# Kernel tuning notes

Measured on AMD Instinct MI355X. Metric: run time of the kernel, lower is better.

## Reference

```python
import jax, jax.numpy as jnp
import numpy as np

NUM_HEADS = 16
D_MODEL = 1024
NUM_LAYERS = 4
VOCAB = 32000
SEQ_LEN = 1024
BATCH = 4
EPS = 1e-6


def position_embedding(seq_len, d_model):
    pos = jnp.arange(seq_len, dtype=jnp.float32)[:, None]
    i = jnp.arange(d_model, dtype=jnp.float32)[None, :]
    # faithful to source: angle_rates = 1 / (1/10000)^(2*(i//2)/d) = 10000^(2*(i//2)/d)
    angle_rates = jnp.power(10000.0, 2.0 * jnp.floor(i / 2.0) / float(d_model))
    ang = pos * angle_rates  # [S, D]
    return jnp.concatenate([jnp.sin(ang[:, 0::2]), jnp.cos(ang[:, 1::2])], axis=-1)[None]  # [1,S,D]


def layer_norm(x, g, b):
    m = jnp.mean(x, axis=-1, keepdims=True)
    v = jnp.mean(jnp.square(x - m), axis=-1, keepdims=True)
    return (x - m) * jax.lax.rsqrt(v + EPS) * g + b


def setup_inputs() -> dict:
    key = jax.random.key(0)
    ks = jax.random.split(key, 20)
    L, D = NUM_LAYERS, D_MODEL
    s = 0.02
    inp = {
        "x": jax.random.randint(ks[0], (BATCH, SEQ_LEN), 0, VOCAB, dtype=jnp.int32),
        "mask": jnp.zeros((BATCH, 1, 1, SEQ_LEN), dtype=jnp.float32),
        "emb": jax.random.normal(ks[1], (VOCAB, D), dtype=jnp.float32) * s,
        "wq": jax.random.normal(ks[2], (L, D, D), dtype=jnp.float32) * s,
        "bq": jnp.zeros((L, D), dtype=jnp.float32),
        "wk": jax.random.normal(ks[3], (L, D, D), dtype=jnp.float32) * s,
        "bk": jnp.zeros((L, D), dtype=jnp.float32),
        "wv": jax.random.normal(ks[4], (L, D, D), dtype=jnp.float32) * s,
        "bv": jnp.zeros((L, D), dtype=jnp.float32),
        "wo": jax.random.normal(ks[5], (L, D, D), dtype=jnp.float32) * s,
        "bo": jnp.zeros((L, D), dtype=jnp.float32),
        "wf": jax.random.normal(ks[6], (L, D, D), dtype=jnp.float32) * s,
        "bf": jnp.zeros((L, D), dtype=jnp.float32),
        "g1": jnp.ones((L, D), dtype=jnp.float32),
        "b1": jnp.zeros((L, D), dtype=jnp.float32),
        "g2": jnp.ones((L, D), dtype=jnp.float32),
        "b2": jnp.zeros((L, D), dtype=jnp.float32),
    }
    return inp


def encoder_forward(x, mask, emb, wq, bq, wk, bk, wv, bv, wo, bo, wf, bf, g1, b1, g2, b2):
    B, S = x.shape
    D = emb.shape[1]
    H = NUM_HEADS
    dh = D // H
    h = emb[x] * jnp.sqrt(jnp.float32(D))  # [B,S,D]
    h = h + position_embedding(S, D)[:, :S, :]

    def split_heads(t):  # [B,S,D] -> [B,H,S,dh]
        return t.reshape(B, S, H, dh).transpose(0, 2, 1, 3)

    for l in range(wq.shape[0]):
        q = split_heads(h @ wq[l] + bq[l])
        k = split_heads(h @ wk[l] + bk[l])
        v = split_heads(h @ wv[l] + bv[l])
        scores = jnp.einsum("bhqd,bhkd->bhqk", q, k) / jnp.sqrt(jnp.float32(dh))
        scores = scores + mask * -1e9
        w = jax.nn.softmax(scores, axis=-1)
        ctx = jnp.einsum("bhqk,bhkd->bhqd", w, v)  # [B,H,S,dh]
        ctx = ctx.transpose(0, 2, 1, 3).reshape(B, S, D)
        attn_out = ctx @ wo[l] + bo[l]
        h = layer_norm(h + attn_out, g1[l], b1[l])
        ff = h @ wf[l] + bf[l]
        h = layer_norm(h + ff, g2[l], b2[l])
    return h


def reference(x, mask, emb, wq, bq, wk, bk, wv, bv, wo, bo, wf, bf, g1, b1, g2, b2):
    return encoder_forward(x, mask, emb, wq, bq, wk, bk, wv, bv, wo, bo, wf, bf, g1, b1, g2, b2)
```

## Files before the change

kernel.cpp:

```cpp
#include <hip/hip_runtime.h>
#include <hip/hip_bf16.h>
#include <math.h>

typedef __hip_bfloat16 bf16;
typedef unsigned int u32;
typedef __attribute__((ext_vector_type(8))) short short8;
typedef __attribute__((ext_vector_type(4))) float f32x4;


#define ATT_LDK 72
#define PS_LD  72

typedef __attribute__((address_space(3))) u32 lds_u32;
typedef const __attribute__((address_space(1))) u32 glb_u32;
static __device__ __forceinline__ void g2l16(const void* g, void* l) {
    __builtin_amdgcn_global_load_lds((glb_u32*)g, (lds_u32*)l, 16, 0, 0);
}

static __device__ __forceinline__ unsigned short bf16bits(float f) {
    bf16 h = __float2bfloat16(f);
    return *(unsigned short*)&h;
}

__global__ __launch_bounds__(256) void wprep_kernel(
    const float* __restrict__ wq, const float* __restrict__ wk,
    const float* __restrict__ wv, const float* __restrict__ wo,
    const float* __restrict__ wf, bf16* __restrict__ wt_all)
{
    __shared__ bf16 tile[64][ATT_LDK];
    const int z = blockIdx.z;
    const int l = z / 5, f = z % 5;
    const float* src = (f == 0) ? wq : (f == 1) ? wk : (f == 2) ? wv : (f == 3) ? wo : wf;
    src += (size_t)l * 1024 * 1024;
    bf16* dst = wt_all + ((size_t)l * 5 + f) * 1024 * 1024;

    const int k0 = blockIdx.x * 64, n0 = blockIdx.y * 64;
    const int t = threadIdx.x;
#pragma unroll
    for (int rr = 0; rr < 4; ++rr) {
        int slot = t + rr * 256;
        int r = slot >> 4, c = slot & 15;
        float4 v = *(const float4*)(src + (size_t)(k0 + r) * 1024 + n0 + c * 4);
        tile[c * 4 + 0][r] = __float2bfloat16(v.x);
        tile[c * 4 + 1][r] = __float2bfloat16(v.y);
        tile[c * 4 + 2][r] = __float2bfloat16(v.z);
        tile[c * 4 + 3][r] = __float2bfloat16(v.w);
    }
    __syncthreads();
#pragma unroll
    for (int rr = 0; rr < 2; ++rr) {
        int slot = t + rr * 256;
        int n = slot >> 3, c = slot & 7;
        *(uint4*)(dst + (size_t)(n0 + n) * 1024 + k0 + c * 8) = *(const uint4*)&tile[n][c * 8];
    }
}

__global__ void bias_stack_kernel(const float* __restrict__ bq, const float* __restrict__ bk,
                                  const float* __restrict__ bv, float* __restrict__ bqkv)
{
    int i = blockIdx.x * 256 + threadIdx.x;
    if (i < 4 * 3072) {
        int l = i / 3072, c = i % 3072;
        int fam = c >> 10, cc = c & 1023;
        const float* s = (fam == 0) ? bq : (fam == 1) ? bk : bv;
        bqkv[i] = s[l * 1024 + cc];
    }
}

__global__ __launch_bounds__(256) void embed_kernel(
    const int* __restrict__ x, const float* __restrict__ emb,
    float* __restrict__ hf, bf16* __restrict__ hb)
{
    int idx = blockIdx.x * 256 + threadIdx.x;
    int d0 = (idx & 255) * 4;
    int row = idx >> 8;
    int s = row & 1023;
    int tok = x[row];
    float4 e = *(const float4*)(emb + (size_t)tok * 1024 + d0);
    float vv[4] = {e.x, e.y, e.z, e.w};
    float out[4];
#pragma unroll
    for (int j = 0; j < 4; ++j) {
        int d = d0 + j;
        int m = (d < 512) ? d : (d - 512);
        float ex = (float)(2 * m) * (1.0f / 1024.0f);
        float rate = (float)pow(10000.0, (double)ex);
        float ang = (float)s * rate;
        double a = (double)ang;
        float pe = (d < 512) ? (float)sin(a) : (float)cos(a);
        out[j] = vv[j] * 32.0f + pe;
    }
    *(float4*)(hf + (size_t)row * 1024 + d0) = *(float4*)out;
    unsigned short pk[4];
#pragma unroll
    for (int j = 0; j < 4; ++j) pk[j] = bf16bits(out[j]);
    *(uint2*)(hb + (size_t)row * 1024 + d0) = *(uint2*)pk;
}

__global__ __launch_bounds__(256, 2) void gemm_bt_kernel(
    const bf16* __restrict__ A, const bf16* __restrict__ Bt,
    const float* __restrict__ bias,
    float* __restrict__ Cf, bf16* __restrict__ Cb,
    int M, int N, int K)
{
    __shared__ bf16 As[128 * 32];
    __shared__ bf16 Bs[128 * 32];
    __shared__ bf16 Cst[4][16 * PS_LD];
    const int t = threadIdx.x;
    const int lane = t & 63, wave = t >> 6;
    const int wr = wave >> 1, wc = wave & 1;
    const int lidx = lane & 15, quad = lane >> 4;
    const int m0 = blockIdx.x * 128, n0 = blockIdx.y * 128;

    f32x4 acc[4][4];
#pragma unroll
    for (int i = 0; i < 4; ++i)
#pragma unroll
        for (int j = 0; j < 4; ++j) acc[i][j] = (f32x4){0.f, 0.f, 0.f, 0.f};

    const int r0 = wave * 32;
    const int rloc = lane >> 2;
    const int csw = ((lane & 3) ^ ((lane >> 3) & 3)) * 8;
    const bf16* Abase = A  + (size_t)(m0 + r0 + rloc) * K + csw;
    const bf16* Bbase = Bt + (size_t)(n0 + r0 + rloc) * K + csw;
    bf16* AsW = As + r0 * 32;
    bf16* BsW = Bs + r0 * 32;
    const int aslot = (quad ^ ((lidx >> 1) & 3)) * 8;

    for (int k0 = 0; k0 < K; k0 += 32) {
        __syncthreads();
        g2l16(Abase + k0,                  AsW);
        g2l16(Abase + k0 + 16 * (size_t)K, AsW + 16 * 32);
        g2l16(Bbase + k0,                  BsW);
        g2l16(Bbase + k0 + 16 * (size_t)K, BsW + 16 * 32);
        __syncthreads();

        short8 af[4], bfr[4];
#pragma unroll
        for (int i = 0; i < 4; ++i)
            af[i] = *(const short8*)(As + (wr * 64 + i * 16 + lidx) * 32 + aslot);
#pragma unroll
        for (int j = 0; j < 4; ++j)
            bfr[j] = *(const short8*)(Bs + (wc * 64 + j * 16 + lidx) * 32 + aslot);
#pragma unroll
        for (int i = 0; i < 4; ++i)
#pragma unroll
            for (int j = 0; j < 4; ++j)
                acc[i][j] = __builtin_amdgcn_mfma_f32_16x16x32_bf16(af[i], bfr[j], acc[i][j], 0, 0, 0);
    }

    float bvj[4];
#pragma unroll
    for (int j = 0; j < 4; ++j)
        bvj[j] = bias ? bias[n0 + wc * 64 + j * 16 + lidx] : 0.0f;

    if (Cb) {
        const int row16 = lane >> 2, c4 = lane & 3;
#pragma unroll
        for (int i = 0; i < 4; ++i) {
#pragma unroll
            for (int j = 0; j < 4; ++j)
#pragma unroll
                for (int r = 0; r < 4; ++r)
                    Cst[wave][(quad * 4 + r) * PS_LD + j * 16 + lidx] =
                        __float2bfloat16(acc[i][j][r] + bvj[j]);
            bf16* dst = Cb + (size_t)(m0 + wr * 64 + i * 16 + row16) * N + n0 + wc * 64;
            const bf16* srcr = &Cst[wave][row16 * PS_LD];
#pragma unroll
            for (int h = 0; h < 2; ++h)
                *(uint4*)(dst + (c4 + 4 * h) * 8) = *(const uint4*)(srcr + (c4 + 4 * h) * 8);
        }
    } else {
#pragma unroll
        for (int i = 0; i < 4; ++i)
#pragma unroll
            for (int j = 0; j < 4; ++j) {
                int col = n0 + wc * 64 + j * 16 + lidx;
#pragma unroll
                for (int r = 0; r < 4; ++r) {
                    int rowg = m0 + wr * 64 + i * 16 + quad * 4 + r;
                    Cf[(size_t)rowg * N + col] = acc[i][j][r] + bvj[j];
                }
            }
    }
}

__global__ __launch_bounds__(256) void transpose_v_kernel(
    const bf16* __restrict__ QKV, bf16* __restrict__ Vt)
{
    __shared__ bf16 tile[64][ATT_LDK];
    const int t = threadIdx.x;
    const int s0 = blockIdx.x * 64, d0 = blockIdx.y * 64, b = blockIdx.z;
#pragma unroll
    for (int rr = 0; rr < 2; ++rr) {
        int slot = t + rr * 256;
        int sl = slot >> 3, c = slot & 7;
        bf16 tmp[8];
        *(uint4*)tmp = *(const uint4*)(QKV + (size_t)(b * 1024 + s0 + sl) * 3072 + 2048 + d0 + c * 8);
#pragma unroll
        for (int j = 0; j < 8; ++j) tile[c * 8 + j][sl] = tmp[j];
    }
    __syncthreads();
#pragma unroll
    for (int rr = 0; rr < 2; ++rr) {
        int slot = t + rr * 256;
        int dl = slot >> 3, c = slot & 7;
        *(uint4*)(Vt + (size_t)(b * 1024 + d0 + dl) * 1024 + s0 + c * 8) = *(const uint4*)&tile[dl][c * 8];
    }
}

__global__ __launch_bounds__(512, 4) void attention_kernel(
    const bf16* __restrict__ QKV,
    const bf16* __restrict__ Vt,
    const float* __restrict__ mask,
    bf16* __restrict__ ctx)
{
    __shared__ bf16 Ks[64 * 64];
    __shared__ bf16 Vs[64 * 64];
    __shared__ bf16 Ps[8][16 * PS_LD];

    const int t = threadIdx.x, lane = t & 63, wave = t >> 6;
    const int quad = lane >> 4, lidx = lane & 15;
    const int b = blockIdx.x >> 4, hh = blockIdx.x & 15;
    const int q0 = blockIdx.y * 128 + wave * 16;

    const int r8 = lane >> 3;
    const int gc = ((lane & 7) ^ r8) * 8;
    const bf16* kg0 = QKV + (size_t)(b * 1024 + wave * 8 + r8) * 3072 + 1024 + hh * 64 + gc;
    const bf16* vg0 = Vt  + (size_t)(b * 1024 + hh * 64 + wave * 8 + r8) * 1024 + gc;
    bf16* KsW = Ks + wave * 8 * 64;
    bf16* VsW = Vs + wave * 8 * 64;

    short8 qf[2];
    {
        const bf16* qp = QKV + (size_t)(b * 1024 + q0 + lidx) * 3072 + hh * 64;
        qf[0] = *(const short8*)(qp + quad * 8);
        qf[1] = *(const short8*)(qp + 32 + quad * 8);
    }

    f32x4 Oacc[4];
#pragma unroll
    for (int nt = 0; nt < 4; ++nt) Oacc[nt] = (f32x4){0.f, 0.f, 0.f, 0.f};
    float psum[4] = {0.f, 0.f, 0.f, 0.f};

    const int fslot = lidx & 7;

    for (int kt = 0; kt < 16; ++kt) {
        __syncthreads();
        g2l16(kg0 + (size_t)kt * 64 * 3072, KsW);
        g2l16(vg0 + kt * 64, VsW);
        __syncthreads();

        f32x4 sacc[4];
#pragma unroll
        for (int nt = 0; nt < 4; ++nt) sacc[nt] = (f32x4){0.f, 0.f, 0.f, 0.f};
#pragma unroll
        for (int kk = 0; kk < 2; ++kk)
#pragma unroll
            for (int nt = 0; nt < 4; ++nt) {
                short8 kf = *(const short8*)(Ks + (nt * 16 + lidx) * 64 + (((kk * 4 + quad) ^ fslot) * 8));
                sacc[nt] = __builtin_amdgcn_mfma_f32_16x16x32_bf16(qf[kk], kf, sacc[nt], 0, 0, 0);
            }

#pragma unroll
        for (int nt = 0; nt < 4; ++nt) {
            float mv = mask[b * 1024 + kt * 64 + nt * 16 + lidx] * -1e9f;
#pragma unroll
            for (int r = 0; r < 4; ++r) {
                float p = __expf(sacc[nt][r] * 0.125f + mv);
                sacc[nt][r] = p;
                psum[r] += p;
            }
        }

#pragma unroll
        for (int nt = 0; nt < 4; ++nt)
#pragma unroll
            for (int r = 0; r < 4; ++r)
                Ps[wave][(quad * 4 + r) * PS_LD + nt * 16 + lidx] = __float2bfloat16(sacc[nt][r]);

#pragma unroll
        for (int kk = 0; kk < 2; ++kk) {
            short8 pf = *(const short8*)(&Ps[wave][lidx * PS_LD + kk * 32 + quad * 8]);
#pragma unroll
            for (int nt = 0; nt < 4; ++nt) {
                short8 vf = *(const short8*)(Vs + (nt * 16 + lidx) * 64 + (((kk * 4 + quad) ^ fslot) * 8));
                Oacc[nt] = __builtin_amdgcn_mfma_f32_16x16x32_bf16(pf, vf, Oacc[nt], 0, 0, 0);
            }
        }
    }

#pragma unroll
    for (int off = 1; off < 16; off <<= 1)
#pragma unroll
        for (int r = 0; r < 4; ++r)
            psum[r] += __shfl_xor(psum[r], off, 64);
    float linv[4];
#pragma unroll
    for (int r = 0; r < 4; ++r) linv[r] = 1.0f / psum[r];

#pragma unroll
    for (int nt = 0; nt < 4; ++nt)
#pragma unroll
        for (int r = 0; r < 4; ++r)
            Ps[wave][(quad * 4 + r) * PS_LD + nt * 16 + lidx] = __float2bfloat16(Oacc[nt][r] * linv[r]);

    const int row16 = lane >> 2, c4 = lane & 3;
    bf16* dst = ctx + (size_t)(b * 1024 + q0 + row16) * 1024 + hh * 64;
    const bf16* srcr = &Ps[wave][row16 * PS_LD];
#pragma unroll
    for (int h = 0; h < 2; ++h)
        *(uint4*)(dst + (c4 + 4 * h) * 8) = *(const uint4*)(srcr + (c4 + 4 * h) * 8);
}

__global__ __launch_bounds__(256) void add_ln_kernel(
    const float* __restrict__ x, const float* __restrict__ dx,
    const float* __restrict__ g, const float* __restrict__ b,
    float* __restrict__ outf, bf16* __restrict__ outb)
{
    __shared__ float red[4];
    const int row = blockIdx.x;
    const int t = threadIdx.x;
    const int c0 = t * 4;
    float4 xv = *(const float4*)(x + (size_t)row * 1024 + c0);
    float4 dv = *(const float4*)(dx + (size_t)row * 1024 + c0);
    float v[4] = {xv.x + dv.x, xv.y + dv.y, xv.z + dv.z, xv.w + dv.w};
    float s = v[0] + v[1] + v[2] + v[3];
#pragma unroll
    for (int off = 1; off < 64; off <<= 1) s += __shfl_xor(s, off, 64);
    if ((t & 63) == 0) red[t >> 6] = s;
    __syncthreads();
    float mean = (red[0] + red[1] + red[2] + red[3]) * (1.0f / 1024.0f);
    float sq = 0.f;
#pragma unroll
    for (int i = 0; i < 4; ++i) { float d = v[i] - mean; sq += d * d; }
#pragma unroll
    for (int off = 1; off < 64; off <<= 1) sq += __shfl_xor(sq, off, 64);
    __syncthreads();
    if ((t & 63) == 0) red[t >> 6] = sq;
    __syncthreads();
    float var = (red[0] + red[1] + red[2] + red[3]) * (1.0f / 1024.0f);
    float rs = rsqrtf(var + 1e-6f);
    float4 gv = *(const float4*)(g + c0);
    float4 bv = *(const float4*)(b + c0);
    float gg[4] = {gv.x, gv.y, gv.z, gv.w}, bb[4] = {bv.x, bv.y, bv.z, bv.w};
    float o[4];
    unsigned short pk[4];
#pragma unroll
    for (int i = 0; i < 4; ++i) {
        o[i] = (v[i] - mean) * rs * gg[i] + bb[i];
        pk[i] = bf16bits(o[i]);
    }
    *(float4*)(outf + (size_t)row * 1024 + c0) = *(float4*)o;
    *(uint2*)(outb + (size_t)row * 1024 + c0) = *(uint2*)pk;
}

extern "C" void kernel_launch(void* const* d_in, const int* in_sizes, int n_in,
                              void* d_out, int out_size, void* d_ws, size_t ws_size,
                              hipStream_t stream)
{
    const int*   x    = (const int*)d_in[0];
    const float* mask = (const float*)d_in[1];
    const float* emb  = (const float*)d_in[2];
    const float* wq   = (const float*)d_in[3];
    const float* bq   = (const float*)d_in[4];
    const float* wk   = (const float*)d_in[5];
    const float* bk   = (const float*)d_in[6];
    const float* wv   = (const float*)d_in[7];
    const float* bv   = (const float*)d_in[8];
    const float* wo   = (const float*)d_in[9];
    const float* bo   = (const float*)d_in[10];
    const float* wf   = (const float*)d_in[11];
    const float* bfp  = (const float*)d_in[12];
    const float* g1   = (const float*)d_in[13];
    const float* b1   = (const float*)d_in[14];
    const float* g2   = (const float*)d_in[15];
    const float* b2   = (const float*)d_in[16];

    char* ws = (char*)d_ws;
    float* h_f  = (float*)ws;                 ws += 4096ull * 1024 * 4;
    bf16*  h_b  = (bf16*)ws;                  ws += 4096ull * 1024 * 2;
    bf16*  qkv  = (bf16*)ws;                  ws += 4096ull * 3072 * 2;
    bf16*  vt   = (bf16*)ws;                  ws += 4096ull * 1024 * 2;
    bf16*  ctx  = (bf16*)ws;                  ws += 4096ull * 1024 * 2;
    bf16*  wt   = (bf16*)ws;                  ws += 20ull * 1024 * 1024 * 2;
    float* bqkv = (float*)ws;                 ws += 4ull * 3072 * 4;
    float* delta = (float*)qkv;

    wprep_kernel<<<dim3(16, 16, 20), 256, 0, stream>>>(wq, wk, wv, wo, wf, wt);
    bias_stack_kernel<<<dim3(48), 256, 0, stream>>>(bq, bk, bv, bqkv);
    embed_kernel<<<dim3(4096), 256, 0, stream>>>(x, emb, h_f, h_b);

    for (int l = 0; l < 4; ++l) {
        bf16* wt_l = wt + (size_t)l * 5 * 1024 * 1024;
        gemm_bt_kernel<<<dim3(32, 24), 256, 0, stream>>>(
            h_b, wt_l, bqkv + l * 3072, nullptr, qkv, 4096, 3072, 1024);
        transpose_v_kernel<<<dim3(16, 16, 4), 256, 0, stream>>>(qkv, vt);
        attention_kernel<<<dim3(64, 8), 512, 0, stream>>>(qkv, vt, mask, ctx);
        gemm_bt_kernel<<<dim3(32, 8), 256, 0, stream>>>(
            ctx, wt_l + 3ull * 1024 * 1024, bo + l * 1024, delta, nullptr, 4096, 1024, 1024);
        add_ln_kernel<<<dim3(4096), 256, 0, stream>>>(
            h_f, delta, g1 + l * 1024, b1 + l * 1024, h_f, h_b);
        gemm_bt_kernel<<<dim3(32, 8), 256, 0, stream>>>(
            h_b, wt_l + 4ull * 1024 * 1024, bfp + l * 1024, delta, nullptr, 4096, 1024, 1024);
        float* outf = (l == 3) ? (float*)d_out : h_f;
        add_ln_kernel<<<dim3(4096), 256, 0, stream>>>(
            h_f, delta, g2 + l * 1024, b2 + l * 1024, outf, h_b);
    }
    (void)in_sizes; (void)n_in; (void)out_size; (void)ws_size;
}
```

Measured before the change: 824.1 us.

## Fuse V transpose into QKV GEMM, add 64-row GEMM, precompute positional table

The QKV GEMM epilogue now writes the V slice straight into the transposed Vt layout, so the separate transpose kernel and its extra read and write of V go away. The output and FFN projections (N=1024) move to a new 64x128-tile GEMM. This doubles the block count to fill more compute units, at the cost of less reuse per tile. The positional embedding, which uses double-precision pow/sin/cos, is computed once into a 1024x1024 table instead of once per batch row. The main GEMM's occupancy hint rises from 2 to 3 blocks per CU. The transposed V stores are narrow 8-byte strided writes that may coalesce poorly.

```diff
diff --git a/kernel.cpp b/kernel.cpp
--- a/kernel.cpp
+++ b/kernel.cpp
@@ -67,17 +67,11 @@
     }
 }
 
-__global__ __launch_bounds__(256) void embed_kernel(
-    const int* __restrict__ x, const float* __restrict__ emb,
-    float* __restrict__ hf, bf16* __restrict__ hb)
+__global__ __launch_bounds__(256) void pe_kernel(float* __restrict__ pe)
 {
     int idx = blockIdx.x * 256 + threadIdx.x;
     int d0 = (idx & 255) * 4;
-    int row = idx >> 8;
-    int s = row & 1023;
-    int tok = x[row];
-    float4 e = *(const float4*)(emb + (size_t)tok * 1024 + d0);
-    float vv[4] = {e.x, e.y, e.z, e.w};
+    int s = idx >> 8;
     float out[4];
 #pragma unroll
     for (int j = 0; j < 4; ++j) {
@@ -87,9 +81,25 @@
         float rate = (float)pow(10000.0, (double)ex);
         float ang = (float)s * rate;
         double a = (double)ang;
-        float pe = (d < 512) ? (float)sin(a) : (float)cos(a);
-        out[j] = vv[j] * 32.0f + pe;
-    }
+        out[j] = (d < 512) ? (float)sin(a) : (float)cos(a);
+    }
+    *(float4*)(pe + (size_t)s * 1024 + d0) = *(float4*)out;
+}
+
+__global__ __launch_bounds__(256) void embed_kernel(
+    const int* __restrict__ x, const float* __restrict__ emb,
+    const float* __restrict__ pe,
+    float* __restrict__ hf, bf16* __restrict__ hb)
+{
+    int idx = blockIdx.x * 256 + threadIdx.x;
+    int d0 = (idx & 255) * 4;
+    int row = idx >> 8;
+    int s = row & 1023;
+    int tok = x[row];
+    float4 e = *(const float4*)(emb + (size_t)tok * 1024 + d0);
+    float4 p = *(const float4*)(pe + (size_t)s * 1024 + d0);
+    float out[4] = {e.x * 32.0f + p.x, e.y * 32.0f + p.y,
+                    e.z * 32.0f + p.z, e.w * 32.0f + p.w};
     *(float4*)(hf + (size_t)row * 1024 + d0) = *(float4*)out;
     unsigned short pk[4];
 #pragma unroll
@@ -97,10 +107,10 @@
     *(uint2*)(hb + (size_t)row * 1024 + d0) = *(uint2*)pk;
 }
 
-__global__ __launch_bounds__(256, 2) void gemm_bt_kernel(
+__global__ __launch_bounds__(256, 3) void gemm_bt_kernel(
     const bf16* __restrict__ A, const bf16* __restrict__ Bt,
     const float* __restrict__ bias,
-    float* __restrict__ Cf, bf16* __restrict__ Cb,
+    bf16* __restrict__ Cb, bf16* __restrict__ VtOut,
     int M, int N, int K)
 {
     __shared__ bf16 As[128 * 32];
@@ -154,7 +164,23 @@
     for (int j = 0; j < 4; ++j)
         bvj[j] = bias ? bias[n0 + wc * 64 + j * 16 + lidx] : 0.0f;
 
-    if (Cb) {
+    if (VtOut && n0 >= 2048) {
+        const int bidx = m0 >> 10;
+        const int s_base = (m0 & 1023) + wr * 64 + quad * 4;
+        const int d_base = (n0 - 2048) + wc * 64;
+#pragma unroll
+        for (int i = 0; i < 4; ++i)
+#pragma unroll
+            for (int j = 0; j < 4; ++j) {
+                unsigned short pk[4];
+#pragma unroll
+                for (int r = 0; r < 4; ++r)
+                    pk[r] = bf16bits(acc[i][j][r] + bvj[j]);
+                bf16* dst = VtOut + ((size_t)bidx * 1024 + d_base + j * 16 + lidx) * 1024
+                            + s_base + i * 16;
+                *(uint2*)dst = *(const uint2*)pk;
+            }
+    } else {
         const int row16 = lane >> 2, c4 = lane & 3;
 #pragma unroll
         for (int i = 0; i < 4; ++i) {
@@ -170,43 +196,69 @@
             for (int h = 0; h < 2; ++h)
                 *(uint4*)(dst + (c4 + 4 * h) * 8) = *(const uint4*)(srcr + (c4 + 4 * h) * 8);
         }
-    } else {
-#pragma unroll
-        for (int i = 0; i < 4; ++i)
-#pragma unroll
-            for (int j = 0; j < 4; ++j) {
-                int col = n0 + wc * 64 + j * 16 + lidx;
-#pragma unroll
-                for (int r = 0; r < 4; ++r) {
-                    int rowg = m0 + wr * 64 + i * 16 + quad * 4 + r;
-                    Cf[(size_t)rowg * N + col] = acc[i][j][r] + bvj[j];
-                }
+    }
+}
+
+__global__ __launch_bounds__(256, 4) void gemm64_kernel(
+    const bf16* __restrict__ A, const bf16* __restrict__ Bt,
+    const float* __restrict__ bias, float* __restrict__ Cf,
+    int M, int N, int K)
+{
+    __shared__ bf16 As[64 * 32];
+    __shared__ bf16 Bs[128 * 32];
+    const int t = threadIdx.x;
+    const int lane = t & 63, wave = t >> 6;
+    const int wr = wave >> 1, wc = wave & 1;
+    const int lidx = lane & 15, quad = lane >> 4;
+    const int m0 = blockIdx.x * 64, n0 = blockIdx.y * 128;
+
+    f32x4 acc[2][4];
+#pragma unroll
+    for (int i = 0; i < 2; ++i)
+#pragma unroll
+        for (int j = 0; j < 4; ++j) acc[i][j] = (f32x4){0.f, 0.f, 0.f, 0.f};
+
+    const int rloc = lane >> 2;
+    const int csw = ((lane & 3) ^ ((lane >> 3) & 3)) * 8;
+    const bf16* Abase = A  + (size_t)(m0 + wave * 16 + rloc) * K + csw;
+    const bf16* Bbase = Bt + (size_t)(n0 + wave * 32 + rloc) * K + csw;
+    bf16* AsW = As + wave * 16 * 32;
+    bf16* BsW = Bs + wave * 32 * 32;
+    const int aslot = (quad ^ ((lidx >> 1) & 3)) * 8;
+
+    for (int k0 = 0; k0 < K; k0 += 32) {
+        __syncthreads();
+        g2l16(Abase + k0,                  AsW);
+        g2l16(Bbase + k0,                  BsW);
+        g2l16(Bbase + k0 + 16 * (size_t)K, BsW + 16 * 32);
+        __syncthreads();
+
+        short8 af[2], bfr[4];
+#pragma unroll
+        for (int i = 0; i < 2; ++i)
+            af[i] = *(const short8*)(As + (wr * 32 + i * 16 + lidx) * 32 + aslot);
+#pragma unroll
+        for (int j = 0; j < 4; ++j)
+            bfr[j] = *(const short8*)(Bs + (wc * 64 + j * 16 + lidx) * 32 + aslot);
+#pragma unroll
+        for (int i = 0; i < 2; ++i)
+#pragma unroll
+            for (int j = 0; j < 4; ++j)
+                acc[i][j] = __builtin_amdgcn_mfma_f32_16x16x32_bf16(af[i], bfr[j], acc[i][j], 0, 0, 0);
+    }
+
+#pragma unroll
+    for (int i = 0; i < 2; ++i)
+#pragma unroll
+        for (int j = 0; j < 4; ++j) {
+            int col = n0 + wc * 64 + j * 16 + lidx;
+            float bv = bias[col];
+#pragma unroll
+            for (int r = 0; r < 4; ++r) {
+                int rowg = m0 + wr * 32 + i * 16 + quad * 4 + r;
+                Cf[(size_t)rowg * N + col] = acc[i][j][r] + bv;
             }
-    }
-}
-
-__global__ __launch_bounds__(256) void transpose_v_kernel(
-    const bf16* __restrict__ QKV, bf16* __restrict__ Vt)
-{
-    __shared__ bf16 tile[64][ATT_LDK];
-    const int t = threadIdx.x;
-    const int s0 = blockIdx.x * 64, d0 = blockIdx.y * 64, b = blockIdx.z;
-#pragma unroll
-    for (int rr = 0; rr < 2; ++rr) {
-        int slot = t + rr * 256;
-        int sl = slot >> 3, c = slot & 7;
-        bf16 tmp[8];
-        *(uint4*)tmp = *(const uint4*)(QKV + (size_t)(b * 1024 + s0 + sl) * 3072 + 2048 + d0 + c * 8);
-#pragma unroll
-        for (int j = 0; j < 8; ++j) tile[c * 8 + j][sl] = tmp[j];
-    }
-    __syncthreads();
-#pragma unroll
-    for (int rr = 0; rr < 2; ++rr) {
-        int slot = t + rr * 256;
-        int dl = slot >> 3, c = slot & 7;
-        *(uint4*)(Vt + (size_t)(b * 1024 + d0 + dl) * 1024 + s0 + c * 8) = *(const uint4*)&tile[dl][c * 8];
-    }
+        }
 }
 
 __global__ __launch_bounds__(512, 4) void attention_kernel(
@@ -384,25 +436,26 @@
     bf16*  vt   = (bf16*)ws;                  ws += 4096ull * 1024 * 2;
     bf16*  ctx  = (bf16*)ws;                  ws += 4096ull * 1024 * 2;
     bf16*  wt   = (bf16*)ws;                  ws += 20ull * 1024 * 1024 * 2;
+    float* pe   = (float*)ws;                 ws += 1024ull * 1024 * 4;
     float* bqkv = (float*)ws;                 ws += 4ull * 3072 * 4;
     float* delta = (float*)qkv;
 
     wprep_kernel<<<dim3(16, 16, 20), 256, 0, stream>>>(wq, wk, wv, wo, wf, wt);
     bias_stack_kernel<<<dim3(48), 256, 0, stream>>>(bq, bk, bv, bqkv);
-    embed_kernel<<<dim3(4096), 256, 0, stream>>>(x, emb, h_f, h_b);
+    pe_kernel<<<dim3(1024), 256, 0, stream>>>(pe);
+    embed_kernel<<<dim3(4096), 256, 0, stream>>>(x, emb, pe, h_f, h_b);
 
     for (int l = 0; l < 4; ++l) {
         bf16* wt_l = wt + (size_t)l * 5 * 1024 * 1024;
         gemm_bt_kernel<<<dim3(32, 24), 256, 0, stream>>>(
-            h_b, wt_l, bqkv + l * 3072, nullptr, qkv, 4096, 3072, 1024);
-        transpose_v_kernel<<<dim3(16, 16, 4), 256, 0, stream>>>(qkv, vt);
+            h_b, wt_l, bqkv + l * 3072, qkv, vt, 4096, 3072, 1024);
         attention_kernel<<<dim3(64, 8), 512, 0, stream>>>(qkv, vt, mask, ctx);
-        gemm_bt_kernel<<<dim3(32, 8), 256, 0, stream>>>(
-            ctx, wt_l + 3ull * 1024 * 1024, bo + l * 1024, delta, nullptr, 4096, 1024, 1024);
+        gemm64_kernel<<<dim3(64, 8), 256, 0, stream>>>(
+            ctx, wt_l + 3ull * 1024 * 1024, bo + l * 1024, delta, 4096, 1024, 1024);
         add_ln_kernel<<<dim3(4096), 256, 0, stream>>>(
             h_f, delta, g1 + l * 1024, b1 + l * 1024, h_f, h_b);
-        gemm_bt_kernel<<<dim3(32, 8), 256, 0, stream>>>(
-            h_b, wt_l + 4ull * 1024 * 1024, bfp + l * 1024, delta, nullptr, 4096, 1024, 1024);
+        gemm64_kernel<<<dim3(64, 8), 256, 0, stream>>>(
+            h_b, wt_l + 4ull * 1024 * 1024, bfp + l * 1024, delta, 4096, 1024, 1024);
         float* outf = (l == 3) ? (float*)d_out : h_f;
         add_ln_kernel<<<dim3(4096), 256, 0, stream>>>(
             h_f, delta, g2 + l * 1024, b2 + l * 1024, outf, h_b);
```

Result: faster. 782.2 us (-5.1%).
